# Optimization experiments

Measured on AMD Instinct MI355X. Metric: run time of the kernel, lower is better.

Reference implementation:

```python
import jax, jax.numpy as jnp
import numpy as np

DECAY = 0.8
EPS = 1e-05


def setup_inputs() -> dict:
    key = jax.random.key(0)
    k_x, k_e = jax.random.split(key)
    x = jax.random.normal(k_x, (8, 4096, 256), dtype=jnp.float32)
    embed = jax.random.normal(k_e, (8192, 256), dtype=jnp.float32)
    cluster_size = jnp.zeros((8192,), dtype=jnp.float32)
    embed_avg = embed  # buffer initialized as embed.clone()
    return {"x": x, "embed": embed, "cluster_size": cluster_size, "embed_avg": embed_avg}


def reference(x, embed, cluster_size, embed_avg):
    shape = x.shape
    K, d = embed.shape
    flatten = x.reshape(-1, d)  # [N, d]

    dist = -(jnp.sum(flatten * flatten, axis=1, keepdims=True)
             - 2.0 * (flatten @ embed.T)
             + jnp.sum(embed * embed, axis=1)[None, :])  # [N, K]
    embed_ind = jnp.argmax(dist, axis=-1)  # [N]

    quantize = jnp.take(embed, embed_ind, axis=0).reshape(shape)
    embed_ind_out = embed_ind.reshape(shape[:-1])

    # Training-mode EMA update (one_hot sum / one_hot matmul expressed as scatter-adds)
    counts = jnp.zeros((K,), dtype=x.dtype).at[embed_ind].add(1.0)  # embed_onehot.sum(0)
    embed_sum = jnp.zeros((K, d), dtype=x.dtype).at[embed_ind].add(flatten)  # (flatten^T @ onehot)^T

    new_cluster_size = cluster_size * DECAY + counts * (1.0 - DECAY)
    new_embed_avg = embed_avg * DECAY + embed_sum * (1.0 - DECAY)

    smoothed = (new_cluster_size + EPS) / (new_cluster_size.sum() + K * EPS) * new_cluster_size.sum()
    new_embed = new_embed_avg / smoothed[:, None]

    return quantize, embed_ind_out, new_cluster_size, new_embed_avg, new_embed
```

## Files before the change

### kernel.cpp

```cpp
#include <hip/hip_runtime.h>

#define N_ROWS 32768
#define DIM    256
#define KCODES 8192
#define DECAYF 0.8f
#define OMDF   0.2f
#define EPSF   1e-5f

#define Q_OFF    0
#define IND_OFF  8388608
#define CS_OFF   8421376
#define EA_OFF   8429568
#define NE_OFF   10526720


#define WS_E2    0
#define WS_CNT   8192
#define WS_START 16384
#define WS_CUR   24576
#define WS_SUM   40960

typedef _Float16 half8 __attribute__((ext_vector_type(8)));
typedef float floatx16 __attribute__((ext_vector_type(16)));

#define PREP_ROWS 32
__global__ void prep_all_kernel(const float* __restrict__ x,
                                const float* __restrict__ embed,
                                const float* __restrict__ cs,
                                _Float16* __restrict__ Xp,
                                _Float16* __restrict__ Ep,
                                float* __restrict__ out,
                                float* __restrict__ ws) {
  __shared__ __align__(16) _Float16 L[PREP_ROWS][264];
  __shared__ float red[4];
  const int t = threadIdx.x;
  const int bid = blockIdx.x;

  if (bid < 1024) {
    if (bid < 128) {
      unsigned long long* gbest = (unsigned long long*)(out + EA_OFF);
      gbest[bid * 256 + t] = 0ULL;
    } else if (bid < 160) {
      ((int*)(ws + WS_CNT))[(bid - 128) * 256 + t] = 0;
    }
    const int row0 = bid * PREP_ROWS;
    #pragma unroll
    for (int it = 0; it < 8; ++it) {
      int idx = it * 256 + t;
      int r = idx >> 6, q = idx & 63;
      float4 v = *(const float4*)&x[(size_t)(row0 + r) * DIM + q * 4];
      L[r][q * 4 + 0] = (_Float16)v.x;
      L[r][q * 4 + 1] = (_Float16)v.y;
      L[r][q * 4 + 2] = (_Float16)v.z;
      L[r][q * 4 + 3] = (_Float16)v.w;
    }
    __syncthreads();
    #pragma unroll
    for (int it = 0; it < 4; ++it) {
      int idx = it * 256 + t;
      int slot = idx >> 5, r = idx & 31;
      *(float4*)&Xp[((size_t)slot * N_ROWS + row0 + r) * 8] =
          *(const float4*)&L[r][slot * 8];
    }
  } else {
    const int row0 = (bid - 1024) * PREP_ROWS;
    float* e2 = ws + WS_E2;
    #pragma unroll
    for (int it = 0; it < 8; ++it) {
      int idx = it * 256 + t;
      int r = idx >> 6, q = idx & 63;
      float4 v = *(const float4*)&embed[(size_t)(row0 + r) * DIM + q * 4];
      L[r][q * 4 + 0] = (_Float16)v.x;
      L[r][q * 4 + 1] = (_Float16)v.y;
      L[r][q * 4 + 2] = (_Float16)v.z;
      L[r][q * 4 + 3] = (_Float16)v.w;
      float ssq = v.x * v.x + v.y * v.y + v.z * v.z + v.w * v.w;
      #pragma unroll
      for (int o = 32; o; o >>= 1) ssq += __shfl_xor(ssq, o);
      if ((t & 63) == 0) e2[row0 + r] = ssq;
    }
    if (bid == 1024) {
      float s = 0.0f;
      for (int j = t; j < KCODES; j += 256) s += cs[j];
      #pragma unroll
      for (int o = 32; o; o >>= 1) s += __shfl_xor(s, o);
      if ((t & 63) == 0) red[t >> 6] = s;
    }
    __syncthreads();
    if (bid == 1024 && t == 0)
      ws[WS_SUM] = red[0] + red[1] + red[2] + red[3];
    #pragma unroll
    for (int it = 0; it < 4; ++it) {
      int idx = it * 256 + t;
      int slot = idx >> 5, r = idx & 31;
      *(float4*)&Ep[((size_t)slot * KCODES + row0 + r) * 8] =
          *(const float4*)&L[r][slot * 8];
    }
  }
}

__global__ __launch_bounds__(512, 2) void main_kernel(
    const _Float16* __restrict__ Xp, const _Float16* __restrict__ Ep,
    const float* __restrict__ e2, unsigned long long* __restrict__ gbest) {
  const int t = threadIdx.x;
  const int w = t >> 6;
  const int lane = t & 63;
  const int l31 = lane & 31;
  const int h = lane >> 5;
  const int wm = w >> 2;
  const int wn = w & 3;

  const int bid = blockIdx.x;
  const int bi = bid >> 3;
  const int cb = (bid & 7) * 4 + (bi >> 7);
  const int rb = bi & 127;
  const int codes0 = cb * 256;
  const int row0 = rb * 256;

  const _Float16* aB = Ep + ((size_t)h * KCODES + codes0 + wm * 128 + l31) * 8;
  const _Float16* bB = Xp + ((size_t)h * N_ROWS + row0 + wn * 64 + l31) * 8;
  const size_t aStep = (size_t)2 * KCODES * 8;
  const size_t bStep = (size_t)2 * N_ROWS * 8;

  floatx16 acc[4][2];
  #pragma unroll
  for (int ct = 0; ct < 4; ++ct) {
    const int cbase = codes0 + wm * 128 + ct * 32 + 4 * h;
    #pragma unroll
    for (int rq = 0; rq < 4; ++rq) {
      float4 v = *(const float4*)&e2[cbase + rq * 8];
      acc[ct][0][rq * 4 + 0] = -0.5f * v.x;
      acc[ct][0][rq * 4 + 1] = -0.5f * v.y;
      acc[ct][0][rq * 4 + 2] = -0.5f * v.z;
      acc[ct][0][rq * 4 + 3] = -0.5f * v.w;
    }
    acc[ct][1] = acc[ct][0];
  }

  half8 A[2][4], B[2][2];
  #pragma unroll
  for (int p = 0; p < 2; ++p) {
    #pragma unroll
    for (int f = 0; f < 4; ++f)
      A[p][f] = *(const half8*)(aB + (size_t)p * aStep + f * 32 * 8);
    B[p][0] = *(const half8*)(bB + (size_t)p * bStep);
    B[p][1] = *(const half8*)(bB + (size_t)p * bStep + 32 * 8);
  }

  #pragma unroll
  for (int j = 0; j < 16; ++j) {
    const int p = j & 1;
    __builtin_amdgcn_s_setprio(1);
    acc[0][0] = __builtin_amdgcn_mfma_f32_32x32x16_f16(A[p][0], B[p][0], acc[0][0], 0, 0, 0);
    acc[0][1] = __builtin_amdgcn_mfma_f32_32x32x16_f16(A[p][0], B[p][1], acc[0][1], 0, 0, 0);
    acc[1][0] = __builtin_amdgcn_mfma_f32_32x32x16_f16(A[p][1], B[p][0], acc[1][0], 0, 0, 0);
    acc[1][1] = __builtin_amdgcn_mfma_f32_32x32x16_f16(A[p][1], B[p][1], acc[1][1], 0, 0, 0);
    acc[2][0] = __builtin_amdgcn_mfma_f32_32x32x16_f16(A[p][2], B[p][0], acc[2][0], 0, 0, 0);
    acc[2][1] = __builtin_amdgcn_mfma_f32_32x32x16_f16(A[p][2], B[p][1], acc[2][1], 0, 0, 0);
    acc[3][0] = __builtin_amdgcn_mfma_f32_32x32x16_f16(A[p][3], B[p][0], acc[3][0], 0, 0, 0);
    acc[3][1] = __builtin_amdgcn_mfma_f32_32x32x16_f16(A[p][3], B[p][1], acc[3][1], 0, 0, 0);
    __builtin_amdgcn_s_setprio(0);
    if (j + 2 < 16) {
      const size_t ja = (size_t)(j + 2) * aStep;
      const size_t jb = (size_t)(j + 2) * bStep;
      #pragma unroll
      for (int f = 0; f < 4; ++f)
        A[p][f] = *(const half8*)(aB + ja + f * 32 * 8);
      B[p][0] = *(const half8*)(bB + jb);
      B[p][1] = *(const half8*)(bB + jb + 32 * 8);
    }
  }

  #pragma unroll
  for (int rt = 0; rt < 2; ++rt) {
    float best = -3.0e38f;
    int bidx = 0;
    #pragma unroll
    for (int ct = 0; ct < 4; ++ct) {
      const int cbase = codes0 + wm * 128 + ct * 32 + 4 * h;
      #pragma unroll
      for (int r = 0; r < 16; ++r) {
        const int code = cbase + (r & 3) + 8 * (r >> 2);
        float v = acc[ct][rt][r];
        if (v > best || (v == best && code < bidx)) { best = v; bidx = code; }
      }
    }
    unsigned u = __float_as_uint(best);
    u = (u & 0x80000000u) ? ~u : (u | 0x80000000u);
    unsigned long long p =
        ((unsigned long long)u << 32) | (unsigned)(8191 - bidx);
    unsigned long long op = (unsigned long long)__shfl_xor((long long)p, 32);
    if (op > p) p = op;
    if (h == 0)
      atomicMax(&gbest[row0 + wn * 64 + rt * 32 + l31], p);
  }
}

__global__ void decode_count_kernel(const unsigned long long* __restrict__ gbest,
                                    float* __restrict__ out,
                                    int* __restrict__ cnt) {
  int r = blockIdx.x * blockDim.x + threadIdx.x;
  unsigned long long p = gbest[r];
  int k = 8191 - (int)(unsigned)(p & 0xFFFFFFFFull);
  out[IND_OFF + r] = (float)k;
  atomicAdd(&cnt[k], 1);
}

__global__ void prefix_kernel(const int* __restrict__ cnt,
                              int* __restrict__ start,
                              int* __restrict__ cursor) {
  __shared__ int part[1024];
  const int t = threadIdx.x;
  int loc[8];
  int s = 0;
  #pragma unroll
  for (int j = 0; j < 8; ++j) { loc[j] = cnt[t * 8 + j]; s += loc[j]; }
  part[t] = s;
  __syncthreads();
  for (int off = 1; off < 1024; off <<= 1) {
    int v = (t >= off) ? part[t - off] : 0;
    __syncthreads();
    part[t] += v;
    __syncthreads();
  }
  int base = part[t] - s;
  #pragma unroll
  for (int j = 0; j < 8; ++j) {
    start[t * 8 + j] = base;
    cursor[t * 8 + j] = base;
    base += loc[j];
  }
}

__global__ void scatter_rows_kernel(const float* __restrict__ out,
                                    int* __restrict__ cursor,
                                    int* __restrict__ rowlist) {
  int r = blockIdx.x * blockDim.x + threadIdx.x;
  int k = (int)out[IND_OFF + r];
  int pos = atomicAdd(&cursor[k], 1);
  rowlist[pos] = r;
}

__global__ void bucket_final_kernel(const float* __restrict__ x,
                                    const float* __restrict__ cs,
                                    const float* __restrict__ embed_avg,
                                    const int* __restrict__ start,
                                    const int* __restrict__ cnt,
                                    const int* __restrict__ rowlist,
                                    float* __restrict__ out,
                                    const float* __restrict__ ws_sum) {
  const int lane = threadIdx.x & 63;
  const int k = blockIdx.x * 4 + (threadIdx.x >> 6);
  const int s = start[k];
  const int n = cnt[k];
  float4 acc = make_float4(0.f, 0.f, 0.f, 0.f);
  int i = 0;
  for (; i + 2 <= n; i += 2) {
    int r0 = rowlist[s + i];
    int r1 = rowlist[s + i + 1];
    float4 v0 = *(const float4*)&x[(size_t)r0 * DIM + lane * 4];
    float4 v1 = *(const float4*)&x[(size_t)r1 * DIM + lane * 4];
    acc.x += v0.x + v1.x; acc.y += v0.y + v1.y;
    acc.z += v0.z + v1.z; acc.w += v0.w + v1.w;
  }
  if (i < n) {
    int r0 = rowlist[s + i];
    float4 v0 = *(const float4*)&x[(size_t)r0 * DIM + lane * 4];
    acc.x += v0.x; acc.y += v0.y; acc.z += v0.z; acc.w += v0.w;
  }
  const float S = DECAYF * (*ws_sum) + OMDF * (float)N_ROWS;
  const float scale = S / (S + (float)KCODES * EPSF);
  float ncs = cs[k] * DECAYF + (float)n * OMDF;
  if (lane == 0) out[CS_OFF + k] = ncs;
  float4 ea = *(const float4*)&embed_avg[(size_t)k * DIM + lane * 4];
  float4 nea;
  nea.x = ea.x * DECAYF + acc.x * OMDF;
  nea.y = ea.y * DECAYF + acc.y * OMDF;
  nea.z = ea.z * DECAYF + acc.z * OMDF;
  nea.w = ea.w * DECAYF + acc.w * OMDF;
  *(float4*)&out[EA_OFF + (size_t)k * DIM + lane * 4] = nea;
  float inv_sm = 1.0f / ((ncs + EPSF) * scale);
  float4 ne;
  ne.x = nea.x * inv_sm;
  ne.y = nea.y * inv_sm;
  ne.z = nea.z * inv_sm;
  ne.w = nea.w * inv_sm;
  *(float4*)&out[NE_OFF + (size_t)k * DIM + lane * 4] = ne;
}

__global__ void finish_q_kernel(const float* __restrict__ embed,
                                float* __restrict__ out) {
  const int lane = threadIdx.x & 63;
  const int wave = (blockIdx.x * blockDim.x + threadIdx.x) >> 6;
  for (int row = wave; row < N_ROWS; row += 2048) {
    int k = (int)out[IND_OFF + row];
    float4 ev = *(const float4*)&embed[(size_t)k * DIM + lane * 4];
    *(float4*)&out[Q_OFF + (size_t)row * DIM + lane * 4] = ev;
  }
}

extern "C" void kernel_launch(void* const* d_in, const int* in_sizes, int n_in,
                              void* d_out, int out_size, void* d_ws, size_t ws_size,
                              hipStream_t stream) {
  const float* x = (const float*)d_in[0];
  const float* embed = (const float*)d_in[1];
  const float* cs = (const float*)d_in[2];
  const float* ea = (const float*)d_in[3];
  float* out = (float*)d_out;
  float* ws = (float*)d_ws;

  float* e2 = ws + WS_E2;
  int* cnt = (int*)(ws + WS_CNT);
  int* start = (int*)(ws + WS_START);
  int* cursor = (int*)(ws + WS_CUR);
  float* ws_sum = ws + WS_SUM;

  _Float16* Xp = (_Float16*)(out + Q_OFF);
  int* rowlist = (int*)(out + Q_OFF + 4194304);
  unsigned long long* gbest = (unsigned long long*)(out + EA_OFF);
  _Float16* Ep = (_Float16*)(out + EA_OFF + 65536);

  prep_all_kernel<<<1280, 256, 0, stream>>>(x, embed, cs, Xp, Ep, out, ws);
  main_kernel<<<4096, 512, 0, stream>>>(Xp, Ep, e2, gbest);
  decode_count_kernel<<<128, 256, 0, stream>>>(gbest, out, cnt);
  prefix_kernel<<<1, 1024, 0, stream>>>(cnt, start, cursor);
  scatter_rows_kernel<<<128, 256, 0, stream>>>(out, cursor, rowlist);
  bucket_final_kernel<<<2048, 256, 0, stream>>>(x, cs, ea, start, cnt,
                                                rowlist, out, ws_sum);
  finish_q_kernel<<<512, 256, 0, stream>>>(embed, out);
}
```

Before: 407.1 us.

## Make main kernel persistent with codebook tile resident in LDS

The distance GEMM now launches 256 persistent blocks instead of 4096. Each block loads a 256-code slice of the fp16 codebook into LDS once, using global_load_lds, then loops over 16 row tiles and streams X from global memory. This removes the repeated global reloads of codebook fragments and most of the per-block launch and prologue work. The cost is 128 KB of LDS per block, which lowers occupancy, and a serial tile loop per block that may leave latency less well hidden.

```diff
diff --git a/kernel.cpp b/kernel.cpp
--- a/kernel.cpp
+++ b/kernel.cpp
@@ -22,6 +22,10 @@
 
 typedef _Float16 half8 __attribute__((ext_vector_type(8)));
 typedef float floatx16 __attribute__((ext_vector_type(16)));
+
+#define GLOAD16(g, l) __builtin_amdgcn_global_load_lds( \
+    (const __attribute__((address_space(1))) void*)(g), \
+    (__attribute__((address_space(3))) void*)(l), 16, 0, 0)
 
 #define PREP_ROWS 32
 __global__ void prep_all_kernel(const float* __restrict__ x,
@@ -102,6 +106,9 @@
 __global__ __launch_bounds__(512, 2) void main_kernel(
     const _Float16* __restrict__ Xp, const _Float16* __restrict__ Ep,
     const float* __restrict__ e2, unsigned long long* __restrict__ gbest) {
+  __shared__ __align__(16) _Float16 As[32 * 256 * 8];
+  __shared__ __align__(16) float e2s[256];
+
   const int t = threadIdx.x;
   const int w = t >> 6;
   const int lane = t & 63;
@@ -112,87 +119,106 @@
 
   const int bid = blockIdx.x;
   const int bi = bid >> 3;
-  const int cb = (bid & 7) * 4 + (bi >> 7);
-  const int rb = bi & 127;
+  const int cb = (bid & 7) * 4 + (bi >> 3);
+  const int rbg = bi & 7;
   const int codes0 = cb * 256;
-  const int row0 = rb * 256;
-
-  const _Float16* aB = Ep + ((size_t)h * KCODES + codes0 + wm * 128 + l31) * 8;
-  const _Float16* bB = Xp + ((size_t)h * N_ROWS + row0 + wn * 64 + l31) * 8;
-  const size_t aStep = (size_t)2 * KCODES * 8;
-  const size_t bStep = (size_t)2 * N_ROWS * 8;
+  const int rowbase = rbg * 4096;
+
+  #pragma unroll
+  for (int it = 0; it < 16; ++it) {
+    const int idx = it * 512 + t;
+    const int slot = idx >> 8;
+    const int code = idx & 255;
+    GLOAD16(Ep + ((size_t)slot * KCODES + codes0 + code) * 8,
+            &As[(slot * 256 + code) * 8]);
+  }
+  if (t < 64) {
+    float4 v = *(const float4*)&e2[codes0 + t * 4];
+    *(float4*)&e2s[t * 4] = v;
+  }
+  asm volatile("s_waitcnt vmcnt(0) lgkmcnt(0)" ::: "memory");
+  __builtin_amdgcn_s_barrier();
+  __builtin_amdgcn_sched_barrier(0);
+
+  const int aIdx = (h * 256 + wm * 128 + l31) * 8;
 
   floatx16 acc[4][2];
-  #pragma unroll
-  for (int ct = 0; ct < 4; ++ct) {
-    const int cbase = codes0 + wm * 128 + ct * 32 + 4 * h;
-    #pragma unroll
-    for (int rq = 0; rq < 4; ++rq) {
-      float4 v = *(const float4*)&e2[cbase + rq * 8];
-      acc[ct][0][rq * 4 + 0] = -0.5f * v.x;
-      acc[ct][0][rq * 4 + 1] = -0.5f * v.y;
-      acc[ct][0][rq * 4 + 2] = -0.5f * v.z;
-      acc[ct][0][rq * 4 + 3] = -0.5f * v.w;
-    }
-    acc[ct][1] = acc[ct][0];
-  }
-
-  half8 A[2][4], B[2][2];
-  #pragma unroll
-  for (int p = 0; p < 2; ++p) {
-    #pragma unroll
-    for (int f = 0; f < 4; ++f)
-      A[p][f] = *(const half8*)(aB + (size_t)p * aStep + f * 32 * 8);
-    B[p][0] = *(const half8*)(bB + (size_t)p * bStep);
-    B[p][1] = *(const half8*)(bB + (size_t)p * bStep + 32 * 8);
-  }
-
-  #pragma unroll
-  for (int j = 0; j < 16; ++j) {
-    const int p = j & 1;
-    __builtin_amdgcn_s_setprio(1);
-    acc[0][0] = __builtin_amdgcn_mfma_f32_32x32x16_f16(A[p][0], B[p][0], acc[0][0], 0, 0, 0);
-    acc[0][1] = __builtin_amdgcn_mfma_f32_32x32x16_f16(A[p][0], B[p][1], acc[0][1], 0, 0, 0);
-    acc[1][0] = __builtin_amdgcn_mfma_f32_32x32x16_f16(A[p][1], B[p][0], acc[1][0], 0, 0, 0);
-    acc[1][1] = __builtin_amdgcn_mfma_f32_32x32x16_f16(A[p][1], B[p][1], acc[1][1], 0, 0, 0);
-    acc[2][0] = __builtin_amdgcn_mfma_f32_32x32x16_f16(A[p][2], B[p][0], acc[2][0], 0, 0, 0);
-    acc[2][1] = __builtin_amdgcn_mfma_f32_32x32x16_f16(A[p][2], B[p][1], acc[2][1], 0, 0, 0);
-    acc[3][0] = __builtin_amdgcn_mfma_f32_32x32x16_f16(A[p][3], B[p][0], acc[3][0], 0, 0, 0);
-    acc[3][1] = __builtin_amdgcn_mfma_f32_32x32x16_f16(A[p][3], B[p][1], acc[3][1], 0, 0, 0);
-    __builtin_amdgcn_s_setprio(0);
-    if (j + 2 < 16) {
-      const size_t ja = (size_t)(j + 2) * aStep;
-      const size_t jb = (size_t)(j + 2) * bStep;
+
+  #pragma unroll 1
+  for (int tile = 0; tile < 16; ++tile) {
+    const int rows0 = rowbase + tile * 256;
+    const _Float16* bB =
+        Xp + ((size_t)h * N_ROWS + rows0 + wn * 64 + l31) * 8;
+
+    #pragma unroll
+    for (int ct = 0; ct < 4; ++ct) {
+      const int cl = wm * 128 + ct * 32 + 4 * h;
       #pragma unroll
-      for (int f = 0; f < 4; ++f)
-        A[p][f] = *(const half8*)(aB + ja + f * 32 * 8);
-      B[p][0] = *(const half8*)(bB + jb);
-      B[p][1] = *(const half8*)(bB + jb + 32 * 8);
-    }
-  }
-
-  #pragma unroll
-  for (int rt = 0; rt < 2; ++rt) {
-    float best = -3.0e38f;
-    int bidx = 0;
-    #pragma unroll
-    for (int ct = 0; ct < 4; ++ct) {
-      const int cbase = codes0 + wm * 128 + ct * 32 + 4 * h;
+      for (int rq = 0; rq < 4; ++rq) {
+        float4 v = *(const float4*)&e2s[cl + rq * 8];
+        acc[ct][0][rq * 4 + 0] = -0.5f * v.x;
+        acc[ct][0][rq * 4 + 1] = -0.5f * v.y;
+        acc[ct][0][rq * 4 + 2] = -0.5f * v.z;
+        acc[ct][0][rq * 4 + 3] = -0.5f * v.w;
+      }
+      acc[ct][1] = acc[ct][0];
+    }
+
+    half8 A[2][4], B[2][2];
+    #pragma unroll
+    for (int ct = 0; ct < 4; ++ct)
+      A[0][ct] = *(const half8*)&As[aIdx + ct * 32 * 8];
+    B[0][0] = *(const half8*)(bB);
+    B[0][1] = *(const half8*)(bB + 32 * 8);
+
+    #pragma unroll
+    for (int j = 0; j < 16; ++j) {
+      const int p = j & 1;
+      const int q = p ^ 1;
+      if (j < 15) {
+        const int sOff = (2 * (j + 1)) * 256 * 8;
+        #pragma unroll
+        for (int ct = 0; ct < 4; ++ct)
+          A[q][ct] = *(const half8*)&As[aIdx + sOff + ct * 32 * 8];
+        const size_t gOff = (size_t)(2 * (j + 1)) * N_ROWS * 8;
+        B[q][0] = *(const half8*)(bB + gOff);
+        B[q][1] = *(const half8*)(bB + gOff + 32 * 8);
+      }
+      __builtin_amdgcn_s_setprio(1);
+      acc[0][0] = __builtin_amdgcn_mfma_f32_32x32x16_f16(A[p][0], B[p][0], acc[0][0], 0, 0, 0);
+      acc[0][1] = __builtin_amdgcn_mfma_f32_32x32x16_f16(A[p][0], B[p][1], acc[0][1], 0, 0, 0);
+      acc[1][0] = __builtin_amdgcn_mfma_f32_32x32x16_f16(A[p][1], B[p][0], acc[1][0], 0, 0, 0);
+      acc[1][1] = __builtin_amdgcn_mfma_f32_32x32x16_f16(A[p][1], B[p][1], acc[1][1], 0, 0, 0);
+      acc[2][0] = __builtin_amdgcn_mfma_f32_32x32x16_f16(A[p][2], B[p][0], acc[2][0], 0, 0, 0);
+      acc[2][1] = __builtin_amdgcn_mfma_f32_32x32x16_f16(A[p][2], B[p][1], acc[2][1], 0, 0, 0);
+      acc[3][0] = __builtin_amdgcn_mfma_f32_32x32x16_f16(A[p][3], B[p][0], acc[3][0], 0, 0, 0);
+      acc[3][1] = __builtin_amdgcn_mfma_f32_32x32x16_f16(A[p][3], B[p][1], acc[3][1], 0, 0, 0);
+      __builtin_amdgcn_s_setprio(0);
+    }
+
+    #pragma unroll
+    for (int rt = 0; rt < 2; ++rt) {
+      float best = -3.0e38f;
+      int bidx = 0;
       #pragma unroll
-      for (int r = 0; r < 16; ++r) {
-        const int code = cbase + (r & 3) + 8 * (r >> 2);
-        float v = acc[ct][rt][r];
-        if (v > best || (v == best && code < bidx)) { best = v; bidx = code; }
+      for (int ct = 0; ct < 4; ++ct) {
+        const int cbase = codes0 + wm * 128 + ct * 32 + 4 * h;
+        #pragma unroll
+        for (int r = 0; r < 16; ++r) {
+          const int code = cbase + (r & 3) + 8 * (r >> 2);
+          float v = acc[ct][rt][r];
+          if (v > best || (v == best && code < bidx)) { best = v; bidx = code; }
+        }
       }
-    }
-    unsigned u = __float_as_uint(best);
-    u = (u & 0x80000000u) ? ~u : (u | 0x80000000u);
-    unsigned long long p =
-        ((unsigned long long)u << 32) | (unsigned)(8191 - bidx);
-    unsigned long long op = (unsigned long long)__shfl_xor((long long)p, 32);
-    if (op > p) p = op;
-    if (h == 0)
-      atomicMax(&gbest[row0 + wn * 64 + rt * 32 + l31], p);
+      unsigned u = __float_as_uint(best);
+      u = (u & 0x80000000u) ? ~u : (u | 0x80000000u);
+      unsigned long long p =
+          ((unsigned long long)u << 32) | (unsigned)(8191 - bidx);
+      unsigned long long op = (unsigned long long)__shfl_xor((long long)p, 32);
+      if (op > p) p = op;
+      if (h == 0)
+        atomicMax(&gbest[rows0 + wn * 64 + rt * 32 + l31], p);
+    }
   }
 }
 
@@ -321,7 +347,7 @@
   _Float16* Ep = (_Float16*)(out + EA_OFF + 65536);
 
   prep_all_kernel<<<1280, 256, 0, stream>>>(x, embed, cs, Xp, Ep, out, ws);
-  main_kernel<<<4096, 512, 0, stream>>>(Xp, Ep, e2, gbest);
+  main_kernel<<<256, 512, 0, stream>>>(Xp, Ep, e2, gbest);
   decode_count_kernel<<<128, 256, 0, stream>>>(gbest, out, cnt);
   prefix_kernel<<<1, 1024, 0, stream>>>(cnt, start, cursor);
   scatter_rows_kernel<<<128, 256, 0, stream>>>(out, cursor, rowlist);
```

Result: slower. 639.6 us (+57.1%).
